# Performance work log

Hardware: AMD Instinct MI355X
Metric: run time of the kernel (lower is better)

The kernel has to match this reference:

```python
import jax, jax.numpy as jnp
import numpy as np

VOCAB = 32000
EMBED = 512
DEP_SIZE = 64
QKV = 512
B, S = 16, 1024
NEG = -1e10


def setup_inputs() -> dict:
    key = jax.random.key(0)
    ks = jax.random.split(key, 16)
    inputs = jax.random.randint(ks[0], (B, S), 0, VOCAB)
    dependency = jax.random.randint(ks[1], (B, S, S), 0, DEP_SIZE)
    embed_table = jax.random.normal(ks[2], (VOCAB, EMBED), dtype=jnp.float32) * 0.02
    dep_table = jax.random.normal(ks[3], (DEP_SIZE, 1), dtype=jnp.float32) * 0.02
    dep_table = dep_table.at[0].set(0.0)  # padding_idx=0
    sc = 1.0 / np.sqrt(EMBED)
    Wq = jax.random.normal(ks[4], (EMBED, QKV), dtype=jnp.float32) * sc
    bq = jnp.zeros((QKV,), jnp.float32)
    Wk = jax.random.normal(ks[5], (EMBED, QKV), dtype=jnp.float32) * sc
    bk = jnp.zeros((QKV,), jnp.float32)
    Wv = jax.random.normal(ks[6], (EMBED, QKV), dtype=jnp.float32) * sc
    bv = jnp.zeros((QKV,), jnp.float32)
    scv = 1.0 / np.sqrt(QKV)
    W1 = jax.random.normal(ks[7], (QKV, QKV), dtype=jnp.float32) * scv
    b1 = jnp.zeros((QKV,), jnp.float32)
    W2 = jax.random.normal(ks[8], (QKV, QKV), dtype=jnp.float32) * scv
    b2 = jnp.zeros((QKV,), jnp.float32)
    return dict(inputs=inputs, dependency=dependency, embed_table=embed_table,
                dep_table=dep_table, Wq=Wq, bq=bq, Wk=Wk, bk=bk, Wv=Wv, bv=bv,
                W1=W1, b1=b1, W2=W2, b2=b2)


def reference(inputs, dependency, embed_table, dep_table, Wq, bq, Wk, bk, Wv, bv, W1, b1, W2, b2):
    x = jnp.take(embed_table, inputs, axis=0)                  # [B,S,E]
    dep_emb = jnp.take(dep_table, dependency, axis=0)[..., 0]  # [B,S,S]
    q = x @ Wq + bq                                            # [B,S,D]
    k = x @ Wk + bk
    v = x @ Wv + bv
    attn = jnp.einsum('bqd,bkd->bqk', q, k) * dep_emb          # [B,S,S]
    attn = jnp.where(dependency == 0, NEG, attn)
    weights = jax.nn.softmax(attn, axis=-1)
    wm = jnp.einsum('bqk,bkd->bqd', weights, v)                # fused weighted sum
    wm = jnp.tanh(wm @ W1 + b1) @ W2 + b2
    return wm, weights
```

## Files before the change

kernel.cpp:

```cpp
#include <hip/hip_runtime.h>

typedef __attribute__((ext_vector_type(8))) short short8;
typedef __attribute__((ext_vector_type(4))) float floatx4;

__device__ __forceinline__ unsigned short f2b(float f) {
  unsigned int u = __float_as_uint(f);
  unsigned int r = (u + 0x7FFFu + ((u >> 16) & 1u)) >> 16;
  return (unsigned short)r;
}
__device__ __forceinline__ uint4 ld8f(const float* p) {
  float4 a = *(const float4*)p;
  float4 b = *(const float4*)(p + 4);
  uint4 r;
  r.x = (unsigned int)f2b(a.x) | ((unsigned int)f2b(a.y) << 16);
  r.y = (unsigned int)f2b(a.z) | ((unsigned int)f2b(a.w) << 16);
  r.z = (unsigned int)f2b(b.x) | ((unsigned int)f2b(b.y) << 16);
  r.w = (unsigned int)f2b(b.z) | ((unsigned int)f2b(b.w) << 16);
  return r;
}

#define GLL(g, l) __builtin_amdgcn_global_load_lds( \
    (const __attribute__((address_space(1))) unsigned int*)(g), \
    (__attribute__((address_space(3))) unsigned int*)(l), 16, 0, 0)

__device__ __forceinline__ void kloop(const unsigned short* __restrict__ A,
                                      const unsigned short* __restrict__ B,
                                      int K, unsigned short* ldsA, unsigned short* ldsB,
                                      floatx4 (&acc)[4][4])
{
  const int tid = threadIdx.x;
  const int w = tid >> 6, lane = tid & 63;
  const int quad = lane >> 4, l16 = lane & 15;
  const int wy = w >> 1, wx = w & 1;
  const int rs = 32 * w + (lane >> 2);
  const int ks = (lane & 3) * 8;
  const int lo0 = (w * 2) * 512 + lane * 8;
  const int lo1 = lo0 + 512;
  const unsigned short* a0 = A + (size_t)rs * K + ks;
  const unsigned short* a1 = a0 + (size_t)16 * K;
  const unsigned short* b0 = B + (size_t)rs * K + ks;
  const unsigned short* b1 = b0 + (size_t)16 * K;

  for (int k0 = 0; k0 < K; k0 += 32) {
    __syncthreads();
    GLL(a0 + k0, &ldsA[lo0]);
    GLL(a1 + k0, &ldsA[lo1]);
    GLL(b0 + k0, &ldsB[lo0]);
    GLL(b1 + k0, &ldsB[lo1]);
    __syncthreads();
    short8 af[4], bf[4];
#pragma unroll
    for (int i = 0; i < 4; i++)
      af[i] = *(const short8*)&ldsA[(wy * 64 + i * 16 + l16) * 32 + quad * 8];
#pragma unroll
    for (int j = 0; j < 4; j++)
      bf[j] = *(const short8*)&ldsB[(wx * 64 + j * 16 + l16) * 32 + quad * 8];
#pragma unroll
    for (int i = 0; i < 4; i++)
#pragma unroll
      for (int j = 0; j < 4; j++)
        acc[i][j] = __builtin_amdgcn_mfma_f32_16x16x32_bf16(af[i], bf[j], acc[i][j], 0, 0, 0);
  }
}

__global__ __launch_bounds__(256, 2) void gemm_qkv(
    const unsigned short* __restrict__ x,
    const unsigned short* __restrict__ WT,
    const float* __restrict__ bq, const float* __restrict__ bk, const float* __restrict__ bv,
    unsigned short* __restrict__ q, unsigned short* __restrict__ kx, unsigned short* __restrict__ v)
{
  __shared__ unsigned short ldsA[4096], ldsB[4096];
  const int m0 = blockIdx.y * 128, n0 = blockIdx.x * 128;
  floatx4 acc[4][4];
#pragma unroll
  for (int i = 0; i < 4; i++)
#pragma unroll
    for (int j = 0; j < 4; j++) acc[i][j] = (floatx4){0.f, 0.f, 0.f, 0.f};

  kloop(x + (size_t)m0 * 512, WT + (size_t)n0 * 512, 512, ldsA, ldsB, acc);

  const int seg = n0 >> 9, nloc = n0 & 511;
  unsigned short* C = seg == 0 ? q : (seg == 1 ? kx : v);
  const float* bias = seg == 0 ? bq : (seg == 1 ? bk : bv);
  const int lane = threadIdx.x & 63, w = threadIdx.x >> 6;
  const int quad = lane >> 4, l16 = lane & 15, wy = w >> 1, wx = w & 1;
  float bvv[4];
#pragma unroll
  for (int j = 0; j < 4; j++) bvv[j] = bias[nloc + wx * 64 + j * 16 + l16];
#pragma unroll
  for (int i = 0; i < 4; i++)
#pragma unroll
    for (int r = 0; r < 4; r++) {
      int m = m0 + wy * 64 + i * 16 + quad * 4 + r;
      unsigned short* crow = C + (size_t)m * 512 + nloc + wx * 64 + l16;
#pragma unroll
      for (int j = 0; j < 4; j++) crow[j * 16] = f2b(acc[i][j][r] + bvv[j]);
    }
}

template<int CF32, int ACT>
__global__ __launch_bounds__(256, 2) void gemm2(
    const unsigned short* __restrict__ A, const unsigned short* __restrict__ Bt,
    const float* __restrict__ bias, void* __restrict__ Cv,
    int N, int K, long aB, long bB, long cB)
{
  __shared__ unsigned short ldsA[4096], ldsB[4096];
  const int b = blockIdx.z;
  const int m0 = blockIdx.y * 128, n0 = blockIdx.x * 128;
  floatx4 acc[4][4];
#pragma unroll
  for (int i = 0; i < 4; i++)
#pragma unroll
    for (int j = 0; j < 4; j++) acc[i][j] = (floatx4){0.f, 0.f, 0.f, 0.f};

  kloop(A + (size_t)b * aB + (size_t)m0 * K, Bt + (size_t)b * bB + (size_t)n0 * K,
        K, ldsA, ldsB, acc);

  const int lane = threadIdx.x & 63, w = threadIdx.x >> 6;
  const int quad = lane >> 4, l16 = lane & 15, wy = w >> 1, wx = w & 1;
  float bvv[4];
#pragma unroll
  for (int j = 0; j < 4; j++)
    bvv[j] = bias ? bias[n0 + wx * 64 + j * 16 + l16] : 0.f;
  float*          Cf = (float*)Cv          + (size_t)b * cB;
  unsigned short* Ch = (unsigned short*)Cv + (size_t)b * cB;
#pragma unroll
  for (int i = 0; i < 4; i++)
#pragma unroll
    for (int r = 0; r < 4; r++) {
      int m = m0 + wy * 64 + i * 16 + quad * 4 + r;
      size_t base = (size_t)m * N + n0 + wx * 64 + l16;
#pragma unroll
      for (int j = 0; j < 4; j++) {
        float vv = acc[i][j][r] + bvv[j];
        if (ACT == 1) vv = tanhf(vv);
        if (CF32) Cf[base + j * 16] = vv;
        else      Ch[base + j * 16] = f2b(vv);
      }
    }
}

#define CST 132
__global__ __launch_bounds__(256, 2) void score_kernel(
    const unsigned short* __restrict__ Q, const unsigned short* __restrict__ Km,
    const int* __restrict__ dep, const float* __restrict__ dept,
    float* __restrict__ E)
{
  __shared__ union {
    struct { unsigned short a[4096]; unsigned short b[4096]; } s;
    float c[32 * CST];
  } sm;
  __shared__ float dtab[64];
  const int tid = threadIdx.x;
  if (tid < 64) dtab[tid] = dept[tid];

  const int b = blockIdx.z;
  const int m0 = blockIdx.y * 128, n0 = blockIdx.x * 128;
  floatx4 acc[4][4];
#pragma unroll
  for (int i = 0; i < 4; i++)
#pragma unroll
    for (int j = 0; j < 4; j++) acc[i][j] = (floatx4){0.f, 0.f, 0.f, 0.f};

  kloop(Q + (size_t)b * (1024 * 512) + (size_t)m0 * 512,
        Km + (size_t)b * (1024 * 512) + (size_t)n0 * 512,
        512, sm.s.a, sm.s.b, acc);

  const int lane = tid & 63, w = tid >> 6;
  const int quad = lane >> 4, l16 = lane & 15, wy = w >> 1, wx = w & 1;
  const int* depb = dep + (size_t)b * 1024 * 1024;
  float* Eb = E + (size_t)b * 1024 * 1024;
  const int cr = tid >> 3, cb = (tid & 7) * 16;

#pragma unroll
  for (int i = 0; i < 4; i++) {
    __syncthreads();
#pragma unroll
    for (int j = 0; j < 4; j++)
#pragma unroll
      for (int r = 0; r < 4; r++)
        sm.c[(wy * 16 + quad * 4 + r) * CST + wx * 64 + j * 16 + l16] = acc[i][j][r];
    __syncthreads();
    const int m = m0 + (cr >> 4) * 64 + i * 16 + (cr & 15);
    const int* dr = depb + (size_t)m * 1024 + n0 + cb;
    float* er = Eb + (size_t)m * 1024 + n0 + cb;
    const float* crow = &sm.c[cr * CST + cb];
#pragma unroll
    for (int c = 0; c < 4; c++) {
      int4 d = *(const int4*)(dr + c * 4);
      float4 s = *(const float4*)(crow + c * 4);
      float4 e;
      e.x = d.x ? __expf(fminf(fmaxf(s.x * dtab[d.x & 63], -60.f), 60.f)) : 0.f;
      e.y = d.y ? __expf(fminf(fmaxf(s.y * dtab[d.y & 63], -60.f), 60.f)) : 0.f;
      e.z = d.z ? __expf(fminf(fmaxf(s.z * dtab[d.z & 63], -60.f), 60.f)) : 0.f;
      e.w = d.w ? __expf(fminf(fmaxf(s.w * dtab[d.w & 63], -60.f), 60.f)) : 0.f;
      *(float4*)(er + c * 4) = e;
    }
  }
}

__global__ void build_x(const float* __restrict__ embed, const int* __restrict__ inputs,
                        unsigned short* __restrict__ x)
{
  const int row = blockIdx.x * 4 + (threadIdx.x >> 6);
  const int lane = threadIdx.x & 63;
  const float* src = embed + (size_t)inputs[row] * 512 + lane * 8;
  *(uint4*)&x[(size_t)row * 512 + lane * 8] = ld8f(src);
}

__global__ void trans_w(const float* s0, const float* s1, const float* s2,
                        const float* s3, const float* s4, unsigned short* dst)
{
  __shared__ unsigned short tile[32][33];
  const int z = blockIdx.z;
  const float* src = z == 0 ? s0 : z == 1 ? s1 : z == 2 ? s2 : z == 3 ? s3 : s4;
  unsigned short* ob = dst + (size_t)z * 262144;
  int c0 = blockIdx.x * 32, r0 = blockIdx.y * 32;
  int tx = threadIdx.x & 31, ty = threadIdx.x >> 5;
  for (int i = ty; i < 32; i += 8)
    tile[i][tx] = f2b(src[(size_t)(r0 + i) * 512 + (c0 + tx)]);
  __syncthreads();
  for (int i = ty; i < 32; i += 8)
    ob[(size_t)(c0 + i) * 512 + (r0 + tx)] = tile[tx][i];
}

__global__ void trans_v(const unsigned short* __restrict__ in, unsigned short* __restrict__ out)
{
  __shared__ unsigned short tile[32][33];
  const unsigned short* ib = in + (size_t)blockIdx.z * (1024 * 512);
  unsigned short* ob = out + (size_t)blockIdx.z * (512 * 1024);
  int c0 = blockIdx.x * 32, r0 = blockIdx.y * 32;
  int tx = threadIdx.x & 31, ty = threadIdx.x >> 5;
  for (int i = ty; i < 32; i += 8)
    tile[i][tx] = ib[(size_t)(r0 + i) * 512 + (c0 + tx)];
  __syncthreads();
  for (int i = ty; i < 32; i += 8)
    ob[(size_t)(c0 + i) * 1024 + (r0 + tx)] = tile[tx][i];
}

__global__ void normalize_rows(float* __restrict__ wf, unsigned short* __restrict__ wb)
{
  size_t row = blockIdx.x;
  float4* p = (float4*)(wf + row * 1024);
  float4 u = p[threadIdx.x];
  float s = (u.x + u.y) + (u.z + u.w);
#pragma unroll
  for (int d = 1; d < 64; d <<= 1) s += __shfl_xor(s, d);
  __shared__ float acc4[4];
  if ((threadIdx.x & 63) == 0) acc4[threadIdx.x >> 6] = s;
  __syncthreads();
  float tot = (acc4[0] + acc4[1]) + (acc4[2] + acc4[3]);
  float inv = tot > 0.f ? 1.f / tot : 0.f;
  u.x *= inv; u.y *= inv; u.z *= inv; u.w *= inv;
  p[threadIdx.x] = u;
  uint2 pk;
  pk.x = (unsigned int)f2b(u.x) | ((unsigned int)f2b(u.y) << 16);
  pk.y = (unsigned int)f2b(u.z) | ((unsigned int)f2b(u.w) << 16);
  *(uint2*)&wb[row * 1024 + threadIdx.x * 4] = pk;
}

extern "C" void kernel_launch(void* const* d_in, const int* in_sizes, int n_in,
                              void* d_out, int out_size, void* d_ws, size_t ws_size,
                              hipStream_t stream)
{
  const int*   inputs     = (const int*)d_in[0];
  const int*   dependency = (const int*)d_in[1];
  const float* embed      = (const float*)d_in[2];
  const float* dept       = (const float*)d_in[3];
  const float* Wq = (const float*)d_in[4];   const float* bq = (const float*)d_in[5];
  const float* Wk = (const float*)d_in[6];   const float* bk = (const float*)d_in[7];
  const float* Wv = (const float*)d_in[8];   const float* bvv = (const float*)d_in[9];
  const float* W1 = (const float*)d_in[10];  const float* b1 = (const float*)d_in[11];
  const float* W2 = (const float*)d_in[12];  const float* b2 = (const float*)d_in[13];

  float* out  = (float*)d_out;
  float* wout = out + (size_t)8388608;

  unsigned short* ws   = (unsigned short*)d_ws;
  unsigned short* q    = ws;
  unsigned short* kx   = ws + 8388608;
  unsigned short* WTc  = ws + 16777216;
  unsigned short* W1T  = ws + 17563648;
  unsigned short* W2T  = ws + 17825792;
  unsigned short* wbf  = ws;
  unsigned short* h    = ws;

  unsigned short* x    = (unsigned short*)wout;
  unsigned short* v    = (unsigned short*)out;
  unsigned short* vT   = (unsigned short*)out + 8388608;
  unsigned short* wmp  = (unsigned short*)out;

  dim3 blk(256);

  trans_w<<<dim3(16, 16, 5), blk, 0, stream>>>(Wq, Wk, Wv, W1, W2, WTc);
  build_x<<<dim3(4096), blk, 0, stream>>>(embed, inputs, x);

  gemm_qkv<<<dim3(12, 128, 1), blk, 0, stream>>>(x, WTc, bq, bk, bvv, q, kx, v);

  score_kernel<<<dim3(8, 8, 16), blk, 0, stream>>>(q, kx, dependency, dept, wout);

  trans_v<<<dim3(16, 32, 16), blk, 0, stream>>>(v, vT);

  normalize_rows<<<dim3(16384), blk, 0, stream>>>(wout, wbf);

  gemm2<0, 0><<<dim3(4, 8, 16), blk, 0, stream>>>(wbf, vT, nullptr, wmp,
                                                  512, 1024, 1024L * 1024, 512L * 1024, 1024L * 512);
  gemm2<0, 1><<<dim3(4, 128, 1), blk, 0, stream>>>(wmp, W1T, b1, h, 512, 512, 0, 0, 0);
  gemm2<1, 0><<<dim3(4, 128, 1), blk, 0, stream>>>(h, W2T, b2, out, 512, 512, 0, 0, 0);
}
```

Measured before the change: 405.0 us.

## Fuse softmax row sums into score kernel and defer normalization after PV GEMM

The score kernel now accumulates per-row exp sums through shuffle reductions and atomics into a global S buffer. A new PV GEMM reads the unnormalized fp32 exponentials, converts them to bf16 on the fly, and scales each output row by 1/S in its epilogue. The old normalize_rows pass, which also wrote a bf16 copy of the weights, is replaced by a lighter scale-only pass. The score kernel also switches from direct global-to-LDS loads to register-staged loads into padded LDS (stride 40) to reduce bank conflicts. The costs are the extra fp32 read traffic in the PV GEMM, the atomics, and a memset.

```diff
diff --git a/kernel.cpp b/kernel.cpp
--- a/kernel.cpp
+++ b/kernel.cpp
@@ -2,6 +2,9 @@
 
 typedef __attribute__((ext_vector_type(8))) short short8;
 typedef __attribute__((ext_vector_type(4))) float floatx4;
+
+#define LSTR 40
+#define CST 132
 
 __device__ __forceinline__ unsigned short f2b(float f) {
   unsigned int u = __float_as_uint(f);
@@ -64,8 +67,7 @@
 }
 
 __global__ __launch_bounds__(256, 2) void gemm_qkv(
-    const unsigned short* __restrict__ x,
-    const unsigned short* __restrict__ WT,
+    const unsigned short* __restrict__ x, const unsigned short* __restrict__ WT,
     const float* __restrict__ bq, const float* __restrict__ bk, const float* __restrict__ bv,
     unsigned short* __restrict__ q, unsigned short* __restrict__ kx, unsigned short* __restrict__ v)
 {
@@ -101,11 +103,9 @@
 template<int CF32, int ACT>
 __global__ __launch_bounds__(256, 2) void gemm2(
     const unsigned short* __restrict__ A, const unsigned short* __restrict__ Bt,
-    const float* __restrict__ bias, void* __restrict__ Cv,
-    int N, int K, long aB, long bB, long cB)
+    const float* __restrict__ bias, void* __restrict__ Cv, int N, int K)
 {
   __shared__ unsigned short ldsA[4096], ldsB[4096];
-  const int b = blockIdx.z;
   const int m0 = blockIdx.y * 128, n0 = blockIdx.x * 128;
   floatx4 acc[4][4];
 #pragma unroll
@@ -113,8 +113,7 @@
 #pragma unroll
     for (int j = 0; j < 4; j++) acc[i][j] = (floatx4){0.f, 0.f, 0.f, 0.f};
 
-  kloop(A + (size_t)b * aB + (size_t)m0 * K, Bt + (size_t)b * bB + (size_t)n0 * K,
-        K, ldsA, ldsB, acc);
+  kloop(A + (size_t)m0 * K, Bt + (size_t)n0 * K, K, ldsA, ldsB, acc);
 
   const int lane = threadIdx.x & 63, w = threadIdx.x >> 6;
   const int quad = lane >> 4, l16 = lane & 15, wy = w >> 1, wx = w & 1;
@@ -122,8 +121,8 @@
 #pragma unroll
   for (int j = 0; j < 4; j++)
     bvv[j] = bias ? bias[n0 + wx * 64 + j * 16 + l16] : 0.f;
-  float*          Cf = (float*)Cv          + (size_t)b * cB;
-  unsigned short* Ch = (unsigned short*)Cv + (size_t)b * cB;
+  float*          Cf = (float*)Cv;
+  unsigned short* Ch = (unsigned short*)Cv;
 #pragma unroll
   for (int i = 0; i < 4; i++)
 #pragma unroll
@@ -140,14 +139,13 @@
     }
 }
 
-#define CST 132
 __global__ __launch_bounds__(256, 2) void score_kernel(
     const unsigned short* __restrict__ Q, const unsigned short* __restrict__ Km,
     const int* __restrict__ dep, const float* __restrict__ dept,
-    float* __restrict__ E)
+    float* __restrict__ E, float* __restrict__ S)
 {
   __shared__ union {
-    struct { unsigned short a[4096]; unsigned short b[4096]; } s;
+    struct { unsigned short a[128 * LSTR]; unsigned short b[128 * LSTR]; } s;
     float c[32 * CST];
   } sm;
   __shared__ float dtab[64];
@@ -155,21 +153,47 @@
   if (tid < 64) dtab[tid] = dept[tid];
 
   const int b = blockIdx.z;
+  const unsigned short* Ab = Q + (size_t)b * (1024 * 512);
+  const unsigned short* Bb = Km + (size_t)b * (1024 * 512);
   const int m0 = blockIdx.y * 128, n0 = blockIdx.x * 128;
-  floatx4 acc[4][4];
-#pragma unroll
-  for (int i = 0; i < 4; i++)
-#pragma unroll
-    for (int j = 0; j < 4; j++) acc[i][j] = (floatx4){0.f, 0.f, 0.f, 0.f};
-
-  kloop(Q + (size_t)b * (1024 * 512) + (size_t)m0 * 512,
-        Km + (size_t)b * (1024 * 512) + (size_t)n0 * 512,
-        512, sm.s.a, sm.s.b, acc);
-
   const int lane = tid & 63, w = tid >> 6;
   const int quad = lane >> 4, l16 = lane & 15, wy = w >> 1, wx = w & 1;
+  const int r0 = tid >> 2, s0 = (tid & 3) * 8;
+
+  floatx4 acc[4][4];
+#pragma unroll
+  for (int i = 0; i < 4; i++)
+#pragma unroll
+    for (int j = 0; j < 4; j++) acc[i][j] = (floatx4){0.f, 0.f, 0.f, 0.f};
+
+  for (int k0 = 0; k0 < 512; k0 += 32) {
+    uint4 av0 = *(const uint4*)(Ab + (size_t)(m0 + r0) * 512 + k0 + s0);
+    uint4 av1 = *(const uint4*)(Ab + (size_t)(m0 + r0 + 64) * 512 + k0 + s0);
+    uint4 bv0 = *(const uint4*)(Bb + (size_t)(n0 + r0) * 512 + k0 + s0);
+    uint4 bv1 = *(const uint4*)(Bb + (size_t)(n0 + r0 + 64) * 512 + k0 + s0);
+    __syncthreads();
+    *(uint4*)&sm.s.a[r0 * LSTR + s0] = av0;
+    *(uint4*)&sm.s.a[(r0 + 64) * LSTR + s0] = av1;
+    *(uint4*)&sm.s.b[r0 * LSTR + s0] = bv0;
+    *(uint4*)&sm.s.b[(r0 + 64) * LSTR + s0] = bv1;
+    __syncthreads();
+    short8 af[4], bf[4];
+#pragma unroll
+    for (int i = 0; i < 4; i++)
+      af[i] = *(const short8*)&sm.s.a[(wy * 64 + i * 16 + l16) * LSTR + quad * 8];
+#pragma unroll
+    for (int j = 0; j < 4; j++)
+      bf[j] = *(const short8*)&sm.s.b[(wx * 64 + j * 16 + l16) * LSTR + quad * 8];
+#pragma unroll
+    for (int i = 0; i < 4; i++)
+#pragma unroll
+      for (int j = 0; j < 4; j++)
+        acc[i][j] = __builtin_amdgcn_mfma_f32_16x16x32_bf16(af[i], bf[j], acc[i][j], 0, 0, 0);
+  }
+
   const int* depb = dep + (size_t)b * 1024 * 1024;
   float* Eb = E + (size_t)b * 1024 * 1024;
+  float* Sb = S + (size_t)b * 1024;
   const int cr = tid >> 3, cb = (tid & 7) * 16;
 
 #pragma unroll
@@ -185,6 +209,7 @@
     const int* dr = depb + (size_t)m * 1024 + n0 + cb;
     float* er = Eb + (size_t)m * 1024 + n0 + cb;
     const float* crow = &sm.c[cr * CST + cb];
+    float ts = 0.f;
 #pragma unroll
     for (int c = 0; c < 4; c++) {
       int4 d = *(const int4*)(dr + c * 4);
@@ -195,8 +220,84 @@
       e.z = d.z ? __expf(fminf(fmaxf(s.z * dtab[d.z & 63], -60.f), 60.f)) : 0.f;
       e.w = d.w ? __expf(fminf(fmaxf(s.w * dtab[d.w & 63], -60.f), 60.f)) : 0.f;
       *(float4*)(er + c * 4) = e;
+      ts += (e.x + e.y) + (e.z + e.w);
     }
+#pragma unroll
+    for (int d = 1; d < 8; d <<= 1) ts += __shfl_xor(ts, d);
+    if ((tid & 7) == 0) atomicAdd(&Sb[m], ts);
   }
+}
+
+__global__ __launch_bounds__(256, 2) void gemm_pv(
+    const float* __restrict__ E, const unsigned short* __restrict__ vT,
+    const float* __restrict__ S, unsigned short* __restrict__ wmp)
+{
+  __shared__ unsigned short ldsA[128 * LSTR];
+  __shared__ unsigned short ldsB[128 * LSTR];
+  const int b = blockIdx.z;
+  const float* Ab = E + (size_t)b * (1024 * 1024);
+  const unsigned short* Bb = vT + (size_t)b * (512 * 1024);
+  const int m0 = blockIdx.y * 128, n0 = blockIdx.x * 128;
+  const int tid = threadIdx.x;
+  const int lane = tid & 63, w = tid >> 6;
+  const int quad = lane >> 4, l16 = lane & 15, wy = w >> 1, wx = w & 1;
+  const int r0 = tid >> 2, s0 = (tid & 3) * 8;
+
+  floatx4 acc[4][4];
+#pragma unroll
+  for (int i = 0; i < 4; i++)
+#pragma unroll
+    for (int j = 0; j < 4; j++) acc[i][j] = (floatx4){0.f, 0.f, 0.f, 0.f};
+
+  for (int k0 = 0; k0 < 1024; k0 += 32) {
+    uint4 av0 = ld8f(Ab + (size_t)(m0 + r0) * 1024 + k0 + s0);
+    uint4 av1 = ld8f(Ab + (size_t)(m0 + r0 + 64) * 1024 + k0 + s0);
+    uint4 bv0 = *(const uint4*)(Bb + (size_t)(n0 + r0) * 1024 + k0 + s0);
+    uint4 bv1 = *(const uint4*)(Bb + (size_t)(n0 + r0 + 64) * 1024 + k0 + s0);
+    __syncthreads();
+    *(uint4*)&ldsA[r0 * LSTR + s0] = av0;
+    *(uint4*)&ldsA[(r0 + 64) * LSTR + s0] = av1;
+    *(uint4*)&ldsB[r0 * LSTR + s0] = bv0;
+    *(uint4*)&ldsB[(r0 + 64) * LSTR + s0] = bv1;
+    __syncthreads();
+    short8 af[4], bf[4];
+#pragma unroll
+    for (int i = 0; i < 4; i++)
+      af[i] = *(const short8*)&ldsA[(wy * 64 + i * 16 + l16) * LSTR + quad * 8];
+#pragma unroll
+    for (int j = 0; j < 4; j++)
+      bf[j] = *(const short8*)&ldsB[(wx * 64 + j * 16 + l16) * LSTR + quad * 8];
+#pragma unroll
+    for (int i = 0; i < 4; i++)
+#pragma unroll
+      for (int j = 0; j < 4; j++)
+        acc[i][j] = __builtin_amdgcn_mfma_f32_16x16x32_bf16(af[i], bf[j], acc[i][j], 0, 0, 0);
+  }
+
+  const float* Sb = S + (size_t)b * 1024;
+  unsigned short* Cb = wmp + (size_t)b * (1024 * 512);
+#pragma unroll
+  for (int i = 0; i < 4; i++)
+#pragma unroll
+    for (int r = 0; r < 4; r++) {
+      int m = m0 + wy * 64 + i * 16 + quad * 4 + r;
+      float sv = Sb[m];
+      float is = sv > 0.f ? 1.f / sv : 0.f;
+      unsigned short* crow = Cb + (size_t)m * 512 + n0 + wx * 64 + l16;
+#pragma unroll
+      for (int j = 0; j < 4; j++) crow[j * 16] = f2b(acc[i][j][r] * is);
+    }
+}
+
+__global__ void scale_rows(float* __restrict__ wf, const float* __restrict__ S)
+{
+  size_t row = blockIdx.x;
+  float sv = S[row];
+  float inv = sv > 0.f ? 1.f / sv : 0.f;
+  float4* p = (float4*)(wf + row * 1024);
+  float4 u = p[threadIdx.x];
+  u.x *= inv; u.y *= inv; u.z *= inv; u.w *= inv;
+  p[threadIdx.x] = u;
 }
 
 __global__ void build_x(const float* __restrict__ embed, const int* __restrict__ inputs,
@@ -238,27 +339,6 @@
     ob[(size_t)(c0 + i) * 1024 + (r0 + tx)] = tile[tx][i];
 }
 
-__global__ void normalize_rows(float* __restrict__ wf, unsigned short* __restrict__ wb)
-{
-  size_t row = blockIdx.x;
-  float4* p = (float4*)(wf + row * 1024);
-  float4 u = p[threadIdx.x];
-  float s = (u.x + u.y) + (u.z + u.w);
-#pragma unroll
-  for (int d = 1; d < 64; d <<= 1) s += __shfl_xor(s, d);
-  __shared__ float acc4[4];
-  if ((threadIdx.x & 63) == 0) acc4[threadIdx.x >> 6] = s;
-  __syncthreads();
-  float tot = (acc4[0] + acc4[1]) + (acc4[2] + acc4[3]);
-  float inv = tot > 0.f ? 1.f / tot : 0.f;
-  u.x *= inv; u.y *= inv; u.z *= inv; u.w *= inv;
-  p[threadIdx.x] = u;
-  uint2 pk;
-  pk.x = (unsigned int)f2b(u.x) | ((unsigned int)f2b(u.y) << 16);
-  pk.y = (unsigned int)f2b(u.z) | ((unsigned int)f2b(u.w) << 16);
-  *(uint2*)&wb[row * 1024 + threadIdx.x * 4] = pk;
-}
-
 extern "C" void kernel_launch(void* const* d_in, const int* in_sizes, int n_in,
                               void* d_out, int out_size, void* d_ws, size_t ws_size,
                               hipStream_t stream)
@@ -282,7 +362,7 @@
   unsigned short* WTc  = ws + 16777216;
   unsigned short* W1T  = ws + 17563648;
   unsigned short* W2T  = ws + 17825792;
-  unsigned short* wbf  = ws;
+  float*          S    = (float*)(ws + 18087936);
   unsigned short* h    = ws;
 
   unsigned short* x    = (unsigned short*)wout;
@@ -292,19 +372,20 @@
 
   dim3 blk(256);
 
+  hipMemsetAsync(S, 0, 16384 * sizeof(float), stream);
   trans_w<<<dim3(16, 16, 5), blk, 0, stream>>>(Wq, Wk, Wv, W1, W2, WTc);
   build_x<<<dim3(4096), blk, 0, stream>>>(embed, inputs, x);
 
   gemm_qkv<<<dim3(12, 128, 1), blk, 0, stream>>>(x, WTc, bq, bk, bvv, q, kx, v);
 
-  score_kernel<<<dim3(8, 8, 16), blk, 0, stream>>>(q, kx, dependency, dept, wout);
+  score_kernel<<<dim3(8, 8, 16), blk, 0, stream>>>(q, kx, dependency, dept, wout, S);
 
   trans_v<<<dim3(16, 32, 16), blk, 0, stream>>>(v, vT);
 
-  normalize_rows<<<dim3(16384), blk, 0, stream>>>(wout, wbf);
-
-  gemm2<0, 0><<<dim3(4, 8, 16), blk, 0, stream>>>(wbf, vT, nullptr, wmp,
-                                                  512, 1024, 1024L * 1024, 512L * 1024, 1024L * 512);
-  gemm2<0, 1><<<dim3(4, 128, 1), blk, 0, stream>>>(wmp, W1T, b1, h, 512, 512, 0, 0, 0);
-  gemm2<1, 0><<<dim3(4, 128, 1), blk, 0, stream>>>(h, W2T, b2, out, 512, 512, 0, 0, 0);
-}
+  gemm_pv<<<dim3(4, 8, 16), blk, 0, stream>>>(wout, vT, S, wmp);
+
+  scale_rows<<<dim3(16384), blk, 0, stream>>>(wout, S);
+
+  gemm2<0, 1><<<dim3(4, 128, 1), blk, 0, stream>>>(wmp, W1T, b1, h, 512, 512);
+  gemm2<1, 0><<<dim3(4, 128, 1), blk, 0, stream>>>(h, W2T, b2, out, 512, 512);
+}
```

Result: slower. 423.5 us (+4.6%).
